# Performance work log

Measured on AMD Instinct MI355X. Metric: run time of the kernel, lower is better.

## Reference

```python
import jax, jax.numpy as jnp
import numpy as np

NUM_HEADS = 16

def setup_inputs() -> dict:
    key = jax.random.key(0)
    ks = jax.random.split(key, 7)
    B, S, D = 2, 2048, 1024
    X = jax.random.normal(ks[0], (B, S, D), dtype=jnp.float32)
    s = 1.0 / np.sqrt(D)
    Wq = jax.random.normal(ks[1], (D, D), dtype=jnp.float32) * s
    Wk = jax.random.normal(ks[2], (D, D), dtype=jnp.float32) * s
    Wv = jax.random.normal(ks[3], (D, D), dtype=jnp.float32) * s
    Wo = jax.random.normal(ks[4], (D, D), dtype=jnp.float32) * s
    bo = jnp.zeros((D,), dtype=jnp.float32)
    return {"X": X, "Wq": Wq, "Wk": Wk, "Wv": Wv, "Wo": Wo, "bo": bo}

def reference(X, Wq, Wk, Wv, Wo, bo):
    B, S, D = X.shape
    H = NUM_HEADS
    hd = D // H
    # project and split heads -> [B, H, S, hd]
    def split(t):
        return t.reshape(B, S, H, hd).transpose(0, 2, 1, 3)
    q = split(X @ Wq)
    k = split(X @ Wk)
    v = split(X @ Wv)
    scores = jnp.einsum('bhqd,bhkd->bhqk', q, k) / jnp.sqrt(jnp.float32(hd))
    causal = jnp.tril(jnp.ones((S, S), dtype=bool))
    scores = jnp.where(causal, scores, -jnp.inf)
    weights = jax.nn.softmax(scores, axis=-1)  # dropout p=0 -> identity
    ctx = jnp.einsum('bhqk,bhkd->bhqd', weights, v)
    ctx = ctx.transpose(0, 2, 1, 3).reshape(B, S, D)
    return ctx @ Wo + bo
```

## Files before the change

kernel.cpp:

```cpp
#include <hip/hip_runtime.h>


typedef __attribute__((ext_vector_type(8))) short short8;
typedef __attribute__((ext_vector_type(4))) float floatx4;

__device__ inline unsigned short f2bf(float f) {
  unsigned u = __float_as_uint(f);
  unsigned r = (u + 0x7fffu + ((u >> 16) & 1u)) >> 16;
  return (unsigned short)r;
}

__device__ __forceinline__ void gll16(const unsigned short* g, unsigned short* l) {
  __builtin_amdgcn_global_load_lds(
      (const __attribute__((address_space(1))) unsigned int*)(g),
      (__attribute__((address_space(3))) unsigned int*)(l),
      16, 0, 0);
}

constexpr int B_ = 2, S_ = 2048, D_ = 1024, H_ = 16, HD_ = 64;

__global__ __launch_bounds__(256) void convert_x(
    const float* __restrict__ x, unsigned short* __restrict__ xb)
{
  const size_t i = ((size_t)blockIdx.x * 256 + threadIdx.x) * 8;
  float4 a = *(const float4*)(x + i);
  float4 b = *(const float4*)(x + i + 4);
  short8 o;
  o[0] = (short)f2bf(a.x); o[1] = (short)f2bf(a.y);
  o[2] = (short)f2bf(a.z); o[3] = (short)f2bf(a.w);
  o[4] = (short)f2bf(b.x); o[5] = (short)f2bf(b.y);
  o[6] = (short)f2bf(b.z); o[7] = (short)f2bf(b.w);
  *(short8*)(xb + i) = o;
}

__global__ __launch_bounds__(256) void transpose_convert_w4(
    const float* __restrict__ w0, const float* __restrict__ w1,
    const float* __restrict__ w2, const float* __restrict__ w3,
    unsigned short* __restrict__ wt_base)
{
  const float* src;
  switch (blockIdx.z) {
    case 0: src = w0; break;
    case 1: src = w1; break;
    case 2: src = w2; break;
    default: src = w3; break;
  }
  unsigned short* dst = wt_base + (size_t)blockIdx.z * 1024 * 1024;
  __shared__ unsigned short t[32][33];
  const int bx = blockIdx.x * 32;
  const int by = blockIdx.y * 32;
  const int x = threadIdx.x;
  for (int yy = threadIdx.y; yy < 32; yy += 8)
    t[yy][x] = f2bf(src[(size_t)(by + yy) * 1024 + bx + x]);
  __syncthreads();
  for (int yy = threadIdx.y; yy < 32; yy += 8)
    dst[(size_t)(bx + yy) * 1024 + by + x] = t[x][yy];
}

__global__ __launch_bounds__(256) void transpose_v(
    const unsigned short* __restrict__ Vb, unsigned short* __restrict__ Vt)
{
  __shared__ unsigned short t[32][33];
  const int bh = blockIdx.z;
  const int b = bh >> 4, h = bh & 15;
  const int s0 = blockIdx.x * 32, d0 = blockIdx.y * 32;
  const int x = threadIdx.x;
  for (int yy = threadIdx.y; yy < 32; yy += 8)
    t[yy][x] = Vb[(size_t)(b * 2048 + s0 + yy) * 1024 + h * 64 + d0 + x];
  __syncthreads();
  for (int yy = threadIdx.y; yy < 32; yy += 8)
    Vt[((size_t)bh * 64 + d0 + yy) * 2048 + s0 + x] = t[x][yy];
}

struct GemmAcc { floatx4 a[4][4]; };

__device__ __forceinline__ void gemm256_core(
    const unsigned short* __restrict__ A,
    const unsigned short* __restrict__ Bt,
    int m0, int bn0, int K,
    unsigned short* sA, unsigned short* sB, GemmAcc& acc)
{
  const int tid = threadIdx.x, wave = tid >> 6, lane = tid & 63;
  const int g = lane >> 4, ml = lane & 15;
  const int wm = wave & 1, wn = wave >> 1;

  const unsigned short* ag0 = A + (size_t)(m0 + (tid >> 2)) * K + (tid & 3) * 8;
  const unsigned short* ag1 = ag0 + (size_t)64 * K;
  const unsigned short* bg0 = Bt + (size_t)(bn0 + (tid >> 2)) * K + (tid & 3) * 8;
  const unsigned short* bg1 = bg0 + (size_t)64 * K;
  unsigned short* sAw0 = sA + wave * 512;
  unsigned short* sAw1 = sA + 2048 + wave * 512;
  unsigned short* sBw0 = sB + wave * 512;
  unsigned short* sBw1 = sB + 2048 + wave * 512;

#pragma unroll
  for (int mt = 0; mt < 4; ++mt)
#pragma unroll
    for (int nt = 0; nt < 4; ++nt) acc.a[mt][nt] = (floatx4){0.f, 0.f, 0.f, 0.f};

  for (int k0 = 0; k0 < K; k0 += 32) {
    __syncthreads();
    gll16(ag0 + k0, sAw0);
    gll16(ag1 + k0, sAw1);
    gll16(bg0 + k0, sBw0);
    gll16(bg1 + k0, sBw1);
    __syncthreads();
    short8 af[4], bf[4];
#pragma unroll
    for (int mt = 0; mt < 4; ++mt)
      af[mt] = *(const short8*)(sA + (wm * 64 + mt * 16 + ml) * 32 + g * 8);
#pragma unroll
    for (int nt = 0; nt < 4; ++nt)
      bf[nt] = *(const short8*)(sB + (wn * 64 + nt * 16 + ml) * 32 + g * 8);
#pragma unroll
    for (int mt = 0; mt < 4; ++mt)
#pragma unroll
      for (int nt = 0; nt < 4; ++nt)
        acc.a[mt][nt] = __builtin_amdgcn_mfma_f32_16x16x32_bf16(
            af[mt], bf[nt], acc.a[mt][nt], 0, 0, 0);
  }
}

__global__ __launch_bounds__(256) void gemm256_qkv(
    const unsigned short* __restrict__ A,
    const unsigned short* __restrict__ Bt,
    unsigned short* __restrict__ Qo,
    unsigned short* __restrict__ Ko,
    unsigned short* __restrict__ Vo)
{
  __shared__ unsigned short sA[128 * 32];
  __shared__ unsigned short sB[128 * 32];
  const int m0 = blockIdx.y * 128;
  const int bn0 = blockIdx.x * 128;
  GemmAcc acc;
  gemm256_core(A, Bt, m0, bn0, 1024, sA, sB, acc);

  const int proj = blockIdx.x >> 3;
  unsigned short* out = (proj == 0) ? Qo : (proj == 1) ? Ko : Vo;
  const int col0 = (blockIdx.x & 7) * 128;
  const int tid = threadIdx.x, wave = tid >> 6, lane = tid & 63;
  const int g = lane >> 4, ml = lane & 15;
  const int wm = wave & 1, wn = wave >> 1;
#pragma unroll
  for (int mt = 0; mt < 4; ++mt) {
#pragma unroll
    for (int nt = 0; nt < 4; ++nt) {
      const int col = col0 + wn * 64 + nt * 16 + ml;
#pragma unroll
      for (int r = 0; r < 4; ++r) {
        const int row = m0 + wm * 64 + mt * 16 + g * 4 + r;
        out[(size_t)row * 1024 + col] = f2bf(acc.a[mt][nt][r]);
      }
    }
  }
}

__global__ __launch_bounds__(256) void gemm_wo64(
    const unsigned short* __restrict__ A,
    const unsigned short* __restrict__ Bt,
    const float* __restrict__ bias,
    float* __restrict__ C)
{
  __shared__ unsigned short sA[64 * 32];
  __shared__ unsigned short sB[128 * 32];
  const int K = 1024;
  const int m0 = blockIdx.y * 64;
  const int bn0 = blockIdx.x * 128;
  const int tid = threadIdx.x, wave = tid >> 6, lane = tid & 63;
  const int g = lane >> 4, ml = lane & 15;
  const int wm = wave & 1, wn = wave >> 1;

  const unsigned short* ag =
      A + (size_t)(m0 + wave * 16 + (lane >> 2)) * K + (lane & 3) * 8;
  const unsigned short* bg0 = Bt + (size_t)(bn0 + (tid >> 2)) * K + (tid & 3) * 8;
  const unsigned short* bg1 = bg0 + (size_t)64 * K;
  unsigned short* sAw  = sA + wave * 512;
  unsigned short* sBw0 = sB + wave * 512;
  unsigned short* sBw1 = sB + 2048 + wave * 512;

  floatx4 acc[2][4];
#pragma unroll
  for (int mt = 0; mt < 2; ++mt)
#pragma unroll
    for (int nt = 0; nt < 4; ++nt) acc[mt][nt] = (floatx4){0.f, 0.f, 0.f, 0.f};

  for (int k0 = 0; k0 < K; k0 += 32) {
    __syncthreads();
    gll16(ag + k0, sAw);
    gll16(bg0 + k0, sBw0);
    gll16(bg1 + k0, sBw1);
    __syncthreads();
    short8 af[2], bf[4];
#pragma unroll
    for (int mt = 0; mt < 2; ++mt)
      af[mt] = *(const short8*)(sA + (wm * 32 + mt * 16 + ml) * 32 + g * 8);
#pragma unroll
    for (int nt = 0; nt < 4; ++nt)
      bf[nt] = *(const short8*)(sB + (wn * 64 + nt * 16 + ml) * 32 + g * 8);
#pragma unroll
    for (int mt = 0; mt < 2; ++mt)
#pragma unroll
      for (int nt = 0; nt < 4; ++nt)
        acc[mt][nt] = __builtin_amdgcn_mfma_f32_16x16x32_bf16(
            af[mt], bf[nt], acc[mt][nt], 0, 0, 0);
  }

#pragma unroll
  for (int mt = 0; mt < 2; ++mt) {
#pragma unroll
    for (int nt = 0; nt < 4; ++nt) {
      const int col = bn0 + wn * 64 + nt * 16 + ml;
      const float badd = bias[col];
#pragma unroll
      for (int r = 0; r < 4; ++r) {
        const int row = m0 + wm * 32 + mt * 16 + g * 4 + r;
        C[(size_t)row * 1024 + col] = acc[mt][nt][r] + badd;
      }
    }
  }
}

constexpr int LDP = 72;

__device__ __forceinline__ void attn_tile(
    const short8* aq, const unsigned short* sKV,
    unsigned short* pw, floatx4* acc, float* l,
    const bool diag, const int qrow0, const int kcol0,
    const int g, const int ml)
{
  const unsigned short* sK0 = sKV;
  const unsigned short* sK1 = sKV + 2048;
  const unsigned short* sV0 = sKV + 4096;
  const unsigned short* sV1 = sKV + 6144;
  const float C1 = 0.18033688f;
  const float C2 = -34.6246810f;

  floatx4 s[4];
#pragma unroll
  for (int nb = 0; nb < 4; ++nb) {
    s[nb] = (floatx4){0.f, 0.f, 0.f, 0.f};
    short8 bk0 = *(const short8*)(sK0 + (nb * 16 + ml) * 32 + g * 8);
    s[nb] = __builtin_amdgcn_mfma_f32_16x16x32_bf16(aq[0], bk0, s[nb], 0, 0, 0);
    short8 bk1 = *(const short8*)(sK1 + (nb * 16 + ml) * 32 + g * 8);
    s[nb] = __builtin_amdgcn_mfma_f32_16x16x32_bf16(aq[1], bk1, s[nb], 0, 0, 0);
  }
#pragma unroll
  for (int r = 0; r < 4; ++r) {
    const int qrow = qrow0 + g * 4 + r;
    float rowsum = 0.f;
#pragma unroll
    for (int nb = 0; nb < 4; ++nb) {
      float e = exp2f(fmaf(s[nb][r], C1, C2));
      if (diag && (kcol0 + nb * 16 + ml > qrow)) e = 0.f;
      const unsigned bits = __float_as_uint(e);
      pw[(g * 4 + r) * LDP + nb * 16 + ml] = (unsigned short)(bits >> 16);
      rowsum += __uint_as_float(bits & 0xffff0000u);
    }
    l[r] += rowsum;
  }
#pragma unroll
  for (int st = 0; st < 2; ++st) {
    short8 ap = *(const short8*)(pw + ml * LDP + st * 32 + g * 8);
    const unsigned short* sv = st ? sV1 : sV0;
#pragma unroll
    for (int jd = 0; jd < 4; ++jd) {
      short8 bv = *(const short8*)(sv + (jd * 16 + ml) * 32 + g * 8);
      acc[jd] = __builtin_amdgcn_mfma_f32_16x16x32_bf16(ap, bv, acc[jd], 0, 0, 0);
    }
  }
}

__global__ __launch_bounds__(256) void attn_v4(
    const unsigned short* __restrict__ Q,
    const unsigned short* __restrict__ Kg,
    const unsigned short* __restrict__ Vt,
    unsigned short* __restrict__ CTX)
{
  __shared__ unsigned short sKV[2][4 * 2048];
  __shared__ unsigned short sP[4 * 16 * LDP];

  const int bh = blockIdx.y;
  const int b = bh >> 4, h = bh & 15;
  const int p = blockIdx.x;
  const int qbA = p, qbB = 31 - p;
  const int qA0 = qbA * 64, qB0 = qbB * 64;
  const int tid = threadIdx.x, wave = tid >> 6, lane = tid & 63;
  const int g = lane >> 4, ml = lane & 15;

  const size_t headoff = (size_t)b * S_ * D_ + (size_t)h * HD_;
  const size_t vtoff   = (size_t)bh * HD_ * S_;

  short8 aqA[2], aqB[2];
  {
    const unsigned short* qp =
        Q + headoff + (size_t)(qA0 + wave * 16 + ml) * D_ + g * 8;
    aqA[0] = *(const short8*)qp;
    aqA[1] = *(const short8*)(qp + 32);
  }
  {
    const unsigned short* qp =
        Q + headoff + (size_t)(qB0 + wave * 16 + ml) * D_ + g * 8;
    aqB[0] = *(const short8*)qp;
    aqB[1] = *(const short8*)(qp + 32);
  }

  floatx4 accA[4], accB[4];
#pragma unroll
  for (int jd = 0; jd < 4; ++jd) {
    accA[jd] = (floatx4){0.f, 0.f, 0.f, 0.f};
    accB[jd] = (floatx4){0.f, 0.f, 0.f, 0.f};
  }
  float lA[4] = {0.f, 0.f, 0.f, 0.f};
  float lB[4] = {0.f, 0.f, 0.f, 0.f};

  const unsigned short* kgb =
      Kg + headoff + (size_t)(wave * 16 + (lane >> 2)) * D_ + (lane & 3) * 8;
  const unsigned short* vgb =
      Vt + vtoff + (size_t)(wave * 16 + (lane >> 2)) * S_ + (lane & 3) * 8;
  unsigned short* pw = sP + wave * 16 * LDP;
  const int woff = wave * 512;

  {
    gll16(kgb,      sKV[0] + 0    + woff);
    gll16(kgb + 32, sKV[0] + 2048 + woff);
    gll16(vgb,      sKV[0] + 4096 + woff);
    gll16(vgb + 32, sKV[0] + 6144 + woff);
  }
  __syncthreads();

  for (int kt = 0; kt <= qbB; ++kt) {
    const int cur = kt & 1;
    if (kt < qbB) {
      const int nxt = cur ^ 1;
      const size_t ko = (size_t)(kt + 1) * 64 * D_;
      const int vo = (kt + 1) * 64;
      gll16(kgb + ko,      sKV[nxt] + 0    + woff);
      gll16(kgb + ko + 32, sKV[nxt] + 2048 + woff);
      gll16(vgb + vo,      sKV[nxt] + 4096 + woff);
      gll16(vgb + vo + 32, sKV[nxt] + 6144 + woff);
    }

    attn_tile(aqB, sKV[cur], pw, accB, lB,
              kt == qbB, qB0 + wave * 16, kt * 64, g, ml);
    if (kt <= qbA)
      attn_tile(aqA, sKV[cur], pw, accA, lA,
                kt == qbA, qA0 + wave * 16, kt * 64, g, ml);

    __syncthreads();
  }

#pragma unroll
  for (int r = 0; r < 4; ++r) {
    float la = lA[r];
    la += __shfl_xor(la, 1); la += __shfl_xor(la, 2);
    la += __shfl_xor(la, 4); la += __shfl_xor(la, 8);
    lA[r] = 1.0f / la;
    float lb = lB[r];
    lb += __shfl_xor(lb, 1); lb += __shfl_xor(lb, 2);
    lb += __shfl_xor(lb, 4); lb += __shfl_xor(lb, 8);
    lB[r] = 1.0f / lb;
  }
#pragma unroll
  for (int r = 0; r < 4; ++r) {
    const int rowA = qA0 + wave * 16 + g * 4 + r;
    const int rowB = qB0 + wave * 16 + g * 4 + r;
#pragma unroll
    for (int jd = 0; jd < 4; ++jd) {
      CTX[headoff + (size_t)rowA * D_ + jd * 16 + ml] = f2bf(accA[jd][r] * lA[r]);
      CTX[headoff + (size_t)rowB * D_ + jd * 16 + ml] = f2bf(accB[jd][r] * lB[r]);
    }
  }
}

extern "C" void kernel_launch(void* const* d_in, const int* in_sizes, int n_in,
                              void* d_out, int out_size, void* d_ws, size_t ws_size,
                              hipStream_t stream)
{
  const float* X  = (const float*)d_in[0];
  const float* Wq = (const float*)d_in[1];
  const float* Wk = (const float*)d_in[2];
  const float* Wv = (const float*)d_in[3];
  const float* Wo = (const float*)d_in[4];
  const float* bo = (const float*)d_in[5];

  char* ws = (char*)d_ws;
  const size_t MB = 1024 * 1024;

  unsigned short* Qb  = (unsigned short*)(ws);
  unsigned short* Kb  = (unsigned short*)(ws + 8 * MB);
  unsigned short* Xb  = (unsigned short*)(ws + 16 * MB);
  unsigned short* WT  = (unsigned short*)(ws + 24 * MB);
  unsigned short* WoT = WT + (size_t)3 * 1024 * 1024;
  unsigned short* Vb  = (unsigned short*)d_out;
  unsigned short* Vt  = Xb;

  convert_x<<<2048, 256, 0, stream>>>(X, Xb);
  transpose_convert_w4<<<dim3(32, 32, 4), dim3(32, 8), 0, stream>>>(
      Wq, Wk, Wv, Wo, WT);
  gemm256_qkv<<<dim3(24, 32), 256, 0, stream>>>(Xb, WT, Qb, Kb, Vb);
  transpose_v<<<dim3(64, 2, 32), dim3(32, 8), 0, stream>>>(Vb, Vt);
  attn_v4<<<dim3(16, B_ * H_), 256, 0, stream>>>(Qb, Kb, Vt, Qb);
  gemm_wo64<<<dim3(8, 64), 256, 0, stream>>>(Qb, WoT, bo, (float*)d_out);
}
```

Baseline: 206.1 us.

## Deepen QKV GEMM k-step and drop attention K/V double buffering

The QKV GEMM now stages two 32-wide k slices per barrier pair, so each iteration covers 64 of K and the number of syncthreads per block is halved. The attention kernel replaces its double-buffered K/V prefetch with single-buffered loads that are waited on each tile. This halves attention shared memory, which may allow more resident blocks per CU, but K/V load latency is no longer overlapped with the previous tile's compute.

```diff
diff --git a/kernel.cpp b/kernel.cpp
--- a/kernel.cpp
+++ b/kernel.cpp
@@ -72,55 +72,6 @@
     Vt[((size_t)bh * 64 + d0 + yy) * 2048 + s0 + x] = t[x][yy];
 }
 
-struct GemmAcc { floatx4 a[4][4]; };
-
-__device__ __forceinline__ void gemm256_core(
-    const unsigned short* __restrict__ A,
-    const unsigned short* __restrict__ Bt,
-    int m0, int bn0, int K,
-    unsigned short* sA, unsigned short* sB, GemmAcc& acc)
-{
-  const int tid = threadIdx.x, wave = tid >> 6, lane = tid & 63;
-  const int g = lane >> 4, ml = lane & 15;
-  const int wm = wave & 1, wn = wave >> 1;
-
-  const unsigned short* ag0 = A + (size_t)(m0 + (tid >> 2)) * K + (tid & 3) * 8;
-  const unsigned short* ag1 = ag0 + (size_t)64 * K;
-  const unsigned short* bg0 = Bt + (size_t)(bn0 + (tid >> 2)) * K + (tid & 3) * 8;
-  const unsigned short* bg1 = bg0 + (size_t)64 * K;
-  unsigned short* sAw0 = sA + wave * 512;
-  unsigned short* sAw1 = sA + 2048 + wave * 512;
-  unsigned short* sBw0 = sB + wave * 512;
-  unsigned short* sBw1 = sB + 2048 + wave * 512;
-
-#pragma unroll
-  for (int mt = 0; mt < 4; ++mt)
-#pragma unroll
-    for (int nt = 0; nt < 4; ++nt) acc.a[mt][nt] = (floatx4){0.f, 0.f, 0.f, 0.f};
-
-  for (int k0 = 0; k0 < K; k0 += 32) {
-    __syncthreads();
-    gll16(ag0 + k0, sAw0);
-    gll16(ag1 + k0, sAw1);
-    gll16(bg0 + k0, sBw0);
-    gll16(bg1 + k0, sBw1);
-    __syncthreads();
-    short8 af[4], bf[4];
-#pragma unroll
-    for (int mt = 0; mt < 4; ++mt)
-      af[mt] = *(const short8*)(sA + (wm * 64 + mt * 16 + ml) * 32 + g * 8);
-#pragma unroll
-    for (int nt = 0; nt < 4; ++nt)
-      bf[nt] = *(const short8*)(sB + (wn * 64 + nt * 16 + ml) * 32 + g * 8);
-#pragma unroll
-    for (int mt = 0; mt < 4; ++mt)
-#pragma unroll
-      for (int nt = 0; nt < 4; ++nt)
-        acc.a[mt][nt] = __builtin_amdgcn_mfma_f32_16x16x32_bf16(
-            af[mt], bf[nt], acc.a[mt][nt], 0, 0, 0);
-  }
-}
-
 __global__ __launch_bounds__(256) void gemm256_qkv(
     const unsigned short* __restrict__ A,
     const unsigned short* __restrict__ Bt,
@@ -128,19 +79,59 @@
     unsigned short* __restrict__ Ko,
     unsigned short* __restrict__ Vo)
 {
-  __shared__ unsigned short sA[128 * 32];
-  __shared__ unsigned short sB[128 * 32];
+  __shared__ unsigned short sA[2][128 * 32];
+  __shared__ unsigned short sB[2][128 * 32];
+  const int K = 1024;
   const int m0 = blockIdx.y * 128;
   const int bn0 = blockIdx.x * 128;
-  GemmAcc acc;
-  gemm256_core(A, Bt, m0, bn0, 1024, sA, sB, acc);
+
+  const int tid = threadIdx.x, wave = tid >> 6, lane = tid & 63;
+  const int g = lane >> 4, ml = lane & 15;
+  const int wm = wave & 1, wn = wave >> 1;
+
+  const unsigned short* ag0 = A + (size_t)(m0 + (tid >> 2)) * K + (tid & 3) * 8;
+  const unsigned short* ag1 = ag0 + (size_t)64 * K;
+  const unsigned short* bg0 = Bt + (size_t)(bn0 + (tid >> 2)) * K + (tid & 3) * 8;
+  const unsigned short* bg1 = bg0 + (size_t)64 * K;
+  const int woff = wave * 512;
+
+  floatx4 acc[4][4];
+#pragma unroll
+  for (int mt = 0; mt < 4; ++mt)
+#pragma unroll
+    for (int nt = 0; nt < 4; ++nt) acc[mt][nt] = (floatx4){0.f, 0.f, 0.f, 0.f};
+
+  for (int k0 = 0; k0 < K; k0 += 64) {
+    __syncthreads();
+#pragma unroll
+    for (int t = 0; t < 2; ++t) {
+      gll16(ag0 + k0 + t * 32, sA[t] + woff);
+      gll16(ag1 + k0 + t * 32, sA[t] + 2048 + woff);
+      gll16(bg0 + k0 + t * 32, sB[t] + woff);
+      gll16(bg1 + k0 + t * 32, sB[t] + 2048 + woff);
+    }
+    __syncthreads();
+#pragma unroll
+    for (int t = 0; t < 2; ++t) {
+      short8 af[4], bf[4];
+#pragma unroll
+      for (int mt = 0; mt < 4; ++mt)
+        af[mt] = *(const short8*)(sA[t] + (wm * 64 + mt * 16 + ml) * 32 + g * 8);
+#pragma unroll
+      for (int nt = 0; nt < 4; ++nt)
+        bf[nt] = *(const short8*)(sB[t] + (wn * 64 + nt * 16 + ml) * 32 + g * 8);
+#pragma unroll
+      for (int mt = 0; mt < 4; ++mt)
+#pragma unroll
+        for (int nt = 0; nt < 4; ++nt)
+          acc[mt][nt] = __builtin_amdgcn_mfma_f32_16x16x32_bf16(
+              af[mt], bf[nt], acc[mt][nt], 0, 0, 0);
+    }
+  }
 
   const int proj = blockIdx.x >> 3;
   unsigned short* out = (proj == 0) ? Qo : (proj == 1) ? Ko : Vo;
   const int col0 = (blockIdx.x & 7) * 128;
-  const int tid = threadIdx.x, wave = tid >> 6, lane = tid & 63;
-  const int g = lane >> 4, ml = lane & 15;
-  const int wm = wave & 1, wn = wave >> 1;
 #pragma unroll
   for (int mt = 0; mt < 4; ++mt) {
 #pragma unroll
@@ -149,7 +140,7 @@
 #pragma unroll
       for (int r = 0; r < 4; ++r) {
         const int row = m0 + wm * 64 + mt * 16 + g * 4 + r;
-        out[(size_t)row * 1024 + col] = f2bf(acc.a[mt][nt][r]);
+        out[(size_t)row * 1024 + col] = f2bf(acc[mt][nt][r]);
       }
     }
   }
@@ -223,15 +214,13 @@
 constexpr int LDP = 72;
 
 __device__ __forceinline__ void attn_tile(
-    const short8* aq, const unsigned short* sKV,
+    const short8* aq,
+    const unsigned short* sK0, const unsigned short* sK1,
+    const unsigned short* sV0, const unsigned short* sV1,
     unsigned short* pw, floatx4* acc, float* l,
     const bool diag, const int qrow0, const int kcol0,
     const int g, const int ml)
 {
-  const unsigned short* sK0 = sKV;
-  const unsigned short* sK1 = sKV + 2048;
-  const unsigned short* sV0 = sKV + 4096;
-  const unsigned short* sV1 = sKV + 6144;
   const float C1 = 0.18033688f;
   const float C2 = -34.6246810f;
 
@@ -270,13 +259,14 @@
   }
 }
 
-__global__ __launch_bounds__(256) void attn_v4(
+__global__ __launch_bounds__(256) void attn_v5(
     const unsigned short* __restrict__ Q,
     const unsigned short* __restrict__ Kg,
     const unsigned short* __restrict__ Vt,
     unsigned short* __restrict__ CTX)
 {
-  __shared__ unsigned short sKV[2][4 * 2048];
+  __shared__ unsigned short sK0[64 * 32], sK1[64 * 32];
+  __shared__ unsigned short sV0[64 * 32], sV1[64 * 32];
   __shared__ unsigned short sP[4 * 16 * LDP];
 
   const int bh = blockIdx.y;
@@ -317,36 +307,26 @@
       Kg + headoff + (size_t)(wave * 16 + (lane >> 2)) * D_ + (lane & 3) * 8;
   const unsigned short* vgb =
       Vt + vtoff + (size_t)(wave * 16 + (lane >> 2)) * S_ + (lane & 3) * 8;
+  unsigned short* sk0w = sK0 + wave * 512;
+  unsigned short* sk1w = sK1 + wave * 512;
+  unsigned short* sv0w = sV0 + wave * 512;
+  unsigned short* sv1w = sV1 + wave * 512;
   unsigned short* pw = sP + wave * 16 * LDP;
-  const int woff = wave * 512;
-
-  {
-    gll16(kgb,      sKV[0] + 0    + woff);
-    gll16(kgb + 32, sKV[0] + 2048 + woff);
-    gll16(vgb,      sKV[0] + 4096 + woff);
-    gll16(vgb + 32, sKV[0] + 6144 + woff);
-  }
-  __syncthreads();
 
   for (int kt = 0; kt <= qbB; ++kt) {
-    const int cur = kt & 1;
-    if (kt < qbB) {
-      const int nxt = cur ^ 1;
-      const size_t ko = (size_t)(kt + 1) * 64 * D_;
-      const int vo = (kt + 1) * 64;
-      gll16(kgb + ko,      sKV[nxt] + 0    + woff);
-      gll16(kgb + ko + 32, sKV[nxt] + 2048 + woff);
-      gll16(vgb + vo,      sKV[nxt] + 4096 + woff);
-      gll16(vgb + vo + 32, sKV[nxt] + 6144 + woff);
-    }
-
-    attn_tile(aqB, sKV[cur], pw, accB, lB,
+    __syncthreads();
+    const size_t ko = (size_t)kt * 64 * D_;
+    gll16(kgb + ko, sk0w);
+    gll16(kgb + ko + 32, sk1w);
+    gll16(vgb + kt * 64, sv0w);
+    gll16(vgb + kt * 64 + 32, sv1w);
+    __syncthreads();
+
+    attn_tile(aqB, sK0, sK1, sV0, sV1, pw, accB, lB,
               kt == qbB, qB0 + wave * 16, kt * 64, g, ml);
     if (kt <= qbA)
-      attn_tile(aqA, sKV[cur], pw, accA, lA,
+      attn_tile(aqA, sK0, sK1, sV0, sV1, pw, accA, lA,
                 kt == qbA, qA0 + wave * 16, kt * 64, g, ml);
-
-    __syncthreads();
   }
 
 #pragma unroll
@@ -399,6 +379,6 @@
       Wq, Wk, Wv, Wo, WT);
   gemm256_qkv<<<dim3(24, 32), 256, 0, stream>>>(Xb, WT, Qb, Kb, Vb);
   transpose_v<<<dim3(64, 2, 32), dim3(32, 8), 0, stream>>>(Vb, Vt);
-  attn_v4<<<dim3(16, B_ * H_), 256, 0, stream>>>(Qb, Kb, Vt, Qb);
+  attn_v5<<<dim3(16, B_ * H_), 256, 0, stream>>>(Qb, Kb, Vt, Qb);
   gemm_wo64<<<dim3(8, 64), 256, 0, stream>>>(Qb, WoT, bo, (float*)d_out);
 }
```

Result: no change. 205.9 us (-0.1%).
